# Performance work log

Measured on AMD Instinct MI355X. Metric: run time of the kernel, lower is better.

## Reference

```python
import jax, jax.numpy as jnp
import numpy as np

B, C, H, W = 8, 256, 128, 128  # dim=256 channels, match_factor=2 -> num_matching=128


def setup_inputs() -> dict:
    key = jax.random.key(0)
    k1, k2 = jax.random.split(key)
    x = jax.random.normal(k1, (B, C, H, W), dtype=jnp.float32)
    Ym = jax.random.normal(k2, (B, C, H, W), dtype=jnp.float32)
    return {"x": x, "Ym": Ym, "num_matching": 128}


def _matching(x, Ym, num_matching):
    # x, Ym: (B, C, H, W); flatten spatial -> (B, C, N) with N = H*W
    b, c, h, w = x.shape
    xf = x.reshape(b, c, h * w)
    yf = Ym.reshape(b, c, h * w)
    # pairwise L2 distances between channel vectors: (B, C, C)
    x2 = jnp.sum(xf * xf, axis=-1)
    y2 = jnp.sum(yf * yf, axis=-1)
    d2 = x2[:, :, None] + y2[:, None, :] - 2.0 * jnp.einsum('bin,bjn->bij', xf, yf)
    dist = jnp.sqrt(jnp.maximum(d2, 0.0))
    # topk(k=1, largest=False) == min / argmin over candidates
    topk_values = jnp.min(dist, axis=-1)      # (B, C)
    topk_indices = jnp.argmin(dist, axis=-1)  # (B, C) nearest candidate per input channel
    # keep the num_matching input channels with smallest min-distance, in original order
    order = jnp.argsort(topk_values, axis=1)[:, :num_matching]  # channel ids with rank < num_matching
    sel = jnp.sort(order, axis=1)                               # restore original channel order (masked_select semantics)
    nn_idx = jnp.take_along_axis(topk_indices, sel, axis=1)     # (B, num_matching)
    # batched gather of candidate rows: (B, num_matching, N)
    filt = jnp.take_along_axis(yf, nn_idx[:, :, None], axis=1)
    return filt.reshape(b, num_matching, h, w)


def reference(x, Ym, num_matching):
    return _matching(x, Ym, num_matching)
```

## Files before the change

kernel.cpp:

```cpp
#include <hip/hip_runtime.h>

#define B_  8
#define C_  256
#define N_  16384
#define NM_ 128

typedef _Float16 f16x8 __attribute__((ext_vector_type(8)));
typedef float    f32x4 __attribute__((ext_vector_type(4)));

#define MFMA16(A, Bf, Cc) __builtin_amdgcn_mfma_f32_16x16x32_f16((A), (Bf), (Cc), 0, 0, 0)
#define AS1 __attribute__((address_space(1)))
#define AS3 __attribute__((address_space(3)))

#define CVT(P0, P1, HI, LO, SQ)                           \
    {                                                     \
        float tmp_[8];                                    \
        *(f32x4*)&tmp_[0] = (P0);                         \
        *(f32x4*)&tmp_[4] = (P1);                         \
        _Pragma("unroll")                                 \
        for (int e_ = 0; e_ < 8; ++e_) {                  \
            float v_ = tmp_[e_];                          \
            _Float16 h_ = (_Float16)v_;                   \
            (HI)[e_] = h_;                                \
            (LO)[e_] = (_Float16)(v_ - (float)h_);        \
            (SQ) += v_ * v_;                              \
        }                                                 \
    }

__global__ __launch_bounds__(512)
__attribute__((amdgpu_waves_per_eu(2, 2)))
void gemm_f16_kernel(const float* __restrict__ X,
                     const float* __restrict__ Y,
                     float* __restrict__ Gp,
                     float* __restrict__ x2p,
                     float* __restrict__ y2p,
                     int Kchunk) {
    __shared__ float A_lds[3][256 * 32];
    __shared__ float B_lds[3][128 * 32];

    int cpx = gridDim.x >> 3;
    int lin = (blockIdx.x & 7) * cpx + (blockIdx.x >> 3);

    int jt = lin & 1, b = (lin >> 1) & 7, ks = lin >> 4;
    int k0 = ks * Kchunk;
    int nsteps = Kchunk >> 5;

    int t = threadIdx.x;
    int lane = t & 63;
    int wid = t >> 6;
    int wm = wid >> 1, wn = wid & 1;
    int fr = lane & 15, ug = lane >> 4;

    const float* Xb = X + (size_t)(b * C_) * N_;
    const float* Yb = Y + (size_t)(b * C_ + jt * 128) * N_;

    int lrow = lane >> 3;
    int lchk = lane & 7;
    int lhalf = lchk & 1;
    int luni = lchk >> 1;

    f32x4 acc[4][4] = {};
    float sA[4] = {0.f, 0.f, 0.f, 0.f};
    float sB[4] = {0.f, 0.f, 0.f, 0.f};

    auto issue = [&](int chunk, int sl) {
        int kbase = k0 + chunk * 32;
#pragma unroll
        for (int q = 0; q < 4; ++q) {
            int r = wid * 32 + q * 8 + lrow;
            int kA = ((luni ^ (r & 3)) << 3) + lhalf * 4;
            __builtin_amdgcn_global_load_lds(
                (const AS1 void*)(Xb + (size_t)r * N_ + kbase + kA),
                (AS3 void*)&A_lds[sl][(wid * 32 + q * 8) * 32], 16, 0, 0);
        }
#pragma unroll
        for (int q = 0; q < 2; ++q) {
            int r = wid * 16 + q * 8 + lrow;
            int kB = ((luni ^ (r & 3)) << 3) + lhalf * 4;
            __builtin_amdgcn_global_load_lds(
                (const AS1 void*)(Yb + (size_t)r * N_ + kbase + kB),
                (AS3 void*)&B_lds[sl][(wid * 16 + q * 8) * 32], 16, 0, 0);
        }
    };

    issue(0, 0);
    issue(1, 1);
    asm volatile("s_waitcnt vmcnt(6)" ::: "memory");
    __builtin_amdgcn_s_barrier();
    __builtin_amdgcn_sched_barrier(0);

    for (int i = 0; i < nsteps; ++i) {
        int sl = i % 3;
        if (i + 2 < nsteps) issue(i + 2, (i + 2) % 3);
        __builtin_amdgcn_sched_barrier(0);

        f16x8 aHi[4], aLo[4];
#pragma unroll
        for (int mf = 0; mf < 4; ++mf) {
            int r = wm * 64 + mf * 16 + fr;
            const float* p = &A_lds[sl][r * 32 + ((ug ^ (r & 3)) << 3)];
            f32x4 p0 = *(const f32x4*)p;
            f32x4 p1 = *(const f32x4*)(p + 4);
            CVT(p0, p1, aHi[mf], aLo[mf], sA[mf]);
        }
#pragma unroll
        for (int nf = 0; nf < 4; ++nf) {
            int r = wn * 64 + nf * 16 + fr;
            const float* p = &B_lds[sl][r * 32 + ((ug ^ (r & 3)) << 3)];
            f32x4 q0 = *(const f32x4*)p;
            f32x4 q1 = *(const f32x4*)(p + 4);
            f16x8 bHi, bLo;
            CVT(q0, q1, bHi, bLo, sB[nf]);
            __builtin_amdgcn_s_setprio(1);
            acc[0][nf] = MFMA16(aHi[0], bHi, acc[0][nf]);
            acc[1][nf] = MFMA16(aHi[1], bHi, acc[1][nf]);
            acc[2][nf] = MFMA16(aHi[2], bHi, acc[2][nf]);
            acc[3][nf] = MFMA16(aHi[3], bHi, acc[3][nf]);
            acc[0][nf] = MFMA16(aHi[0], bLo, acc[0][nf]);
            acc[1][nf] = MFMA16(aHi[1], bLo, acc[1][nf]);
            acc[2][nf] = MFMA16(aHi[2], bLo, acc[2][nf]);
            acc[3][nf] = MFMA16(aHi[3], bLo, acc[3][nf]);
            acc[0][nf] = MFMA16(aLo[0], bHi, acc[0][nf]);
            acc[1][nf] = MFMA16(aLo[1], bHi, acc[1][nf]);
            acc[2][nf] = MFMA16(aLo[2], bHi, acc[2][nf]);
            acc[3][nf] = MFMA16(aLo[3], bHi, acc[3][nf]);
            __builtin_amdgcn_s_setprio(0);
        }

        __builtin_amdgcn_sched_barrier(0);
        if (i + 2 < nsteps) {
            asm volatile("s_waitcnt vmcnt(6)" ::: "memory");
        } else {
            asm volatile("s_waitcnt vmcnt(0)" ::: "memory");
        }
        __builtin_amdgcn_s_barrier();
        __builtin_amdgcn_sched_barrier(0);
    }

#pragma unroll
    for (int mf = 0; mf < 4; ++mf) {
        float s = sA[mf];
        s += __shfl_xor(s, 16);
        s += __shfl_xor(s, 32);
        if (jt == 0 && wn == 0 && lane < 16)
            x2p[(ks * B_ + b) * C_ + wm * 64 + mf * 16 + lane] = s;
    }
#pragma unroll
    for (int nf = 0; nf < 4; ++nf) {
        float s = sB[nf];
        s += __shfl_xor(s, 16);
        s += __shfl_xor(s, 32);
        if (wm == 0 && lane < 16)
            y2p[(ks * B_ + b) * C_ + jt * 128 + wn * 64 + nf * 16 + lane] = s;
    }

    size_t gbase = (size_t)(ks * B_ + b) * C_ * C_ + (size_t)jt * 128;
#pragma unroll
    for (int mf = 0; mf < 4; ++mf)
#pragma unroll
        for (int nf = 0; nf < 4; ++nf) {
            int rr = wm * 64 + mf * 16 + (lane >> 4) * 4;
            int cc = wn * 64 + nf * 16 + (lane & 15);
#pragma unroll
            for (int r = 0; r < 4; ++r)
                Gp[gbase + (size_t)(rr + r) * C_ + cc] = acc[mf][nf][r];
        }
}

__global__ __launch_bounds__(256) void argmin_kernel(const float* __restrict__ Gp,
                                                     const float* __restrict__ x2p,
                                                     const float* __restrict__ y2p,
                                                     float* __restrict__ minval,
                                                     int* __restrict__ minidx,
                                                     int KS) {
    int bi = blockIdx.x;
    int b = bi >> 8;
    int i = bi & 255;
    int j = threadIdx.x;

    float g = 0.f, sx = 0.f, sy = 0.f;
    for (int ks = 0; ks < KS; ++ks) {
        g  += Gp[((size_t)(ks * B_ + b) * C_ + i) * C_ + j];
        sx += x2p[(ks * B_ + b) * C_ + i];
        sy += y2p[(ks * B_ + b) * C_ + j];
    }

    float v = sx + sy - 2.f * g;
    int idx = j;
#pragma unroll
    for (int off = 32; off > 0; off >>= 1) {
        float v2 = __shfl_down(v, off);
        int i2 = __shfl_down(idx, off);
        if (v2 < v || (v2 == v && i2 < idx)) { v = v2; idx = i2; }
    }
    __shared__ float wv[4];
    __shared__ int wi[4];
    int lane = threadIdx.x & 63, wid = threadIdx.x >> 6;
    if (lane == 0) { wv[wid] = v; wi[wid] = idx; }
    __syncthreads();
    if (threadIdx.x == 0) {
        for (int w = 1; w < 4; ++w)
            if (wv[w] < v || (wv[w] == v && wi[w] < idx)) { v = wv[w]; idx = wi[w]; }
        minval[bi] = v;
        minidx[bi] = idx;
    }
}

__global__ __launch_bounds__(256) void select_kernel(const float* __restrict__ minval,
                                                     const int* __restrict__ minidx,
                                                     int* __restrict__ nn) {
    int b = blockIdx.x;
    int i = threadIdx.x;
    __shared__ float vals[C_];
    __shared__ int wcnt[4];

    float v = minval[b * C_ + i];
    vals[i] = v;
    __syncthreads();

    int rank = 0;
    for (int tt = 0; tt < C_; ++tt) {
        float u = vals[tt];
        rank += (u < v) || (u == v && tt < i);
    }
    bool flag = rank < NM_;

    unsigned long long m = __ballot(flag);
    int lane = i & 63, wid = i >> 6;
    if (lane == 0) wcnt[wid] = (int)__popcll(m);
    __syncthreads();
    int off = 0;
    for (int w = 0; w < wid; ++w) off += wcnt[w];
    int pos = off + (int)__popcll(m & ((1ULL << lane) - 1ULL));
    if (flag) nn[b * NM_ + pos] = minidx[b * C_ + i];
}

__global__ __launch_bounds__(256) void gather_kernel(const float* __restrict__ Y,
                                                     const int* __restrict__ nn,
                                                     float* __restrict__ out) {
    int blk = blockIdx.x;
    int b = blk >> 7;
    int m = blk & 127;
    int src = nn[b * NM_ + m];
    const float4* s = (const float4*)(Y + ((size_t)b * C_ + src) * N_);
    float4* d = (float4*)(out + ((size_t)b * NM_ + m) * N_);
    for (int tt = threadIdx.x; tt < N_ / 4; tt += 256) d[tt] = s[tt];
}

extern "C" void kernel_launch(void* const* d_in, const int* in_sizes, int n_in,
                              void* d_out, int out_size, void* d_ws, size_t ws_size,
                              hipStream_t stream) {
    const float* X = (const float*)d_in[0];
    const float* Y = (const float*)d_in[1];
    float* out = (float*)d_out;

    size_t favail = ws_size / 4;
    int KS = 1;
    while (KS < 16) {
        int KS2 = KS * 2;
        size_t need = (size_t)KS2 * B_ * C_ * C_
                    + (size_t)KS2 * 2 * B_ * C_
                    + 2 * B_ * C_ + B_ * NM_;
        if (need > favail) break;
        KS = KS2;
    }
    int Kchunk = N_ / KS;

    float* minval = (float*)d_ws;
    int* minidx = (int*)(minval + B_ * C_);
    int* nn = minidx + B_ * C_;
    float* x2p = (float*)(nn + B_ * NM_);
    float* y2p = x2p + (size_t)KS * B_ * C_;
    float* Gp = y2p + (size_t)KS * B_ * C_;

    hipLaunchKernelGGL(gemm_f16_kernel, dim3(KS * 16), dim3(512), 0, stream, X, Y, Gp, x2p, y2p, Kchunk);
    hipLaunchKernelGGL(argmin_kernel, dim3(B_ * C_), dim3(256), 0, stream, Gp, x2p, y2p, minval, minidx, KS);
    hipLaunchKernelGGL(select_kernel, dim3(B_), dim3(256), 0, stream, minval, minidx, nn);
    hipLaunchKernelGGL(gather_kernel, dim3(B_ * NM_), dim3(256), 0, stream, Y, nn, out);
}
```

Baseline: 146.5 us.

## Split GEMM into 128x128 tiles with 256-thread blocks and double buffering

Result: faster. 130.6 us (-10.9%).

```diff
diff --git a/kernel.cpp b/kernel.cpp
--- a/kernel.cpp
+++ b/kernel.cpp
@@ -27,7 +27,7 @@
         }                                                 \
     }
 
-__global__ __launch_bounds__(512)
+__global__ __launch_bounds__(256)
 __attribute__((amdgpu_waves_per_eu(2, 2)))
 void gemm_f16_kernel(const float* __restrict__ X,
                      const float* __restrict__ Y,
@@ -35,13 +35,13 @@
                      float* __restrict__ x2p,
                      float* __restrict__ y2p,
                      int Kchunk) {
-    __shared__ float A_lds[3][256 * 32];
-    __shared__ float B_lds[3][128 * 32];
+    __shared__ float A_lds[2][128 * 32];
+    __shared__ float B_lds[2][128 * 32];
 
     int cpx = gridDim.x >> 3;
     int lin = (blockIdx.x & 7) * cpx + (blockIdx.x >> 3);
 
-    int jt = lin & 1, b = (lin >> 1) & 7, ks = lin >> 4;
+    int jt = lin & 1, it = (lin >> 1) & 1, b = (lin >> 2) & 7, ks = lin >> 5;
     int k0 = ks * Kchunk;
     int nsteps = Kchunk >> 5;
 
@@ -51,13 +51,12 @@
     int wm = wid >> 1, wn = wid & 1;
     int fr = lane & 15, ug = lane >> 4;
 
-    const float* Xb = X + (size_t)(b * C_) * N_;
+    const float* Xb = X + (size_t)(b * C_ + it * 128) * N_;
     const float* Yb = Y + (size_t)(b * C_ + jt * 128) * N_;
 
     int lrow = lane >> 3;
     int lchk = lane & 7;
-    int lhalf = lchk & 1;
-    int luni = lchk >> 1;
+    int lsw = (lchk ^ lrow) << 2;
 
     f32x4 acc[4][4] = {};
     float sA[4] = {0.f, 0.f, 0.f, 0.f};
@@ -68,47 +67,43 @@
 #pragma unroll
         for (int q = 0; q < 4; ++q) {
             int r = wid * 32 + q * 8 + lrow;
-            int kA = ((luni ^ (r & 3)) << 3) + lhalf * 4;
             __builtin_amdgcn_global_load_lds(
-                (const AS1 void*)(Xb + (size_t)r * N_ + kbase + kA),
+                (const AS1 void*)(Xb + (size_t)r * N_ + kbase + lsw),
                 (AS3 void*)&A_lds[sl][(wid * 32 + q * 8) * 32], 16, 0, 0);
         }
 #pragma unroll
-        for (int q = 0; q < 2; ++q) {
-            int r = wid * 16 + q * 8 + lrow;
-            int kB = ((luni ^ (r & 3)) << 3) + lhalf * 4;
+        for (int q = 0; q < 4; ++q) {
+            int r = wid * 32 + q * 8 + lrow;
             __builtin_amdgcn_global_load_lds(
-                (const AS1 void*)(Yb + (size_t)r * N_ + kbase + kB),
-                (AS3 void*)&B_lds[sl][(wid * 16 + q * 8) * 32], 16, 0, 0);
+                (const AS1 void*)(Yb + (size_t)r * N_ + kbase + lsw),
+                (AS3 void*)&B_lds[sl][(wid * 32 + q * 8) * 32], 16, 0, 0);
         }
     };
 
     issue(0, 0);
-    issue(1, 1);
-    asm volatile("s_waitcnt vmcnt(6)" ::: "memory");
+    if (nsteps > 1) issue(1, 1);
+    asm volatile("s_waitcnt vmcnt(8)" ::: "memory");
     __builtin_amdgcn_s_barrier();
     __builtin_amdgcn_sched_barrier(0);
 
     for (int i = 0; i < nsteps; ++i) {
-        int sl = i % 3;
-        if (i + 2 < nsteps) issue(i + 2, (i + 2) % 3);
-        __builtin_amdgcn_sched_barrier(0);
+        int sl = i & 1;
 
         f16x8 aHi[4], aLo[4];
 #pragma unroll
         for (int mf = 0; mf < 4; ++mf) {
             int r = wm * 64 + mf * 16 + fr;
-            const float* p = &A_lds[sl][r * 32 + ((ug ^ (r & 3)) << 3)];
-            f32x4 p0 = *(const f32x4*)p;
-            f32x4 p1 = *(const f32x4*)(p + 4);
+            int s7 = r & 7;
+            f32x4 p0 = *(const f32x4*)&A_lds[sl][r * 32 + (((ug * 2)     ^ s7) << 2)];
+            f32x4 p1 = *(const f32x4*)&A_lds[sl][r * 32 + (((ug * 2 + 1) ^ s7) << 2)];
             CVT(p0, p1, aHi[mf], aLo[mf], sA[mf]);
         }
 #pragma unroll
         for (int nf = 0; nf < 4; ++nf) {
             int r = wn * 64 + nf * 16 + fr;
-            const float* p = &B_lds[sl][r * 32 + ((ug ^ (r & 3)) << 3)];
-            f32x4 q0 = *(const f32x4*)p;
-            f32x4 q1 = *(const f32x4*)(p + 4);
+            int s7 = r & 7;
+            f32x4 q0 = *(const f32x4*)&B_lds[sl][r * 32 + (((ug * 2)     ^ s7) << 2)];
+            f32x4 q1 = *(const f32x4*)&B_lds[sl][r * 32 + (((ug * 2 + 1) ^ s7) << 2)];
             f16x8 bHi, bLo;
             CVT(q0, q1, bHi, bLo, sB[nf]);
             __builtin_amdgcn_s_setprio(1);
@@ -129,12 +124,15 @@
 
         __builtin_amdgcn_sched_barrier(0);
         if (i + 2 < nsteps) {
-            asm volatile("s_waitcnt vmcnt(6)" ::: "memory");
+            asm volatile("s_waitcnt vmcnt(0)" ::: "memory");
+            __builtin_amdgcn_s_barrier();
+            __builtin_amdgcn_sched_barrier(0);
+            issue(i + 2, sl);
         } else {
             asm volatile("s_waitcnt vmcnt(0)" ::: "memory");
-        }
-        __builtin_amdgcn_s_barrier();
-        __builtin_amdgcn_sched_barrier(0);
+            __builtin_amdgcn_s_barrier();
+            __builtin_amdgcn_sched_barrier(0);
+        }
     }
 
 #pragma unroll
@@ -143,18 +141,18 @@
         s += __shfl_xor(s, 16);
         s += __shfl_xor(s, 32);
         if (jt == 0 && wn == 0 && lane < 16)
-            x2p[(ks * B_ + b) * C_ + wm * 64 + mf * 16 + lane] = s;
+            x2p[(ks * B_ + b) * C_ + it * 128 + wm * 64 + mf * 16 + lane] = s;
     }
 #pragma unroll
     for (int nf = 0; nf < 4; ++nf) {
         float s = sB[nf];
         s += __shfl_xor(s, 16);
         s += __shfl_xor(s, 32);
-        if (wm == 0 && lane < 16)
+        if (it == 0 && wm == 0 && lane < 16)
             y2p[(ks * B_ + b) * C_ + jt * 128 + wn * 64 + nf * 16 + lane] = s;
     }
 
-    size_t gbase = (size_t)(ks * B_ + b) * C_ * C_ + (size_t)jt * 128;
+    size_t gbase = ((size_t)(ks * B_ + b) * C_ + it * 128) * C_ + jt * 128;
 #pragma unroll
     for (int mf = 0; mf < 4; ++mf)
 #pragma unroll
@@ -273,7 +271,7 @@
     float* y2p = x2p + (size_t)KS * B_ * C_;
     float* Gp = y2p + (size_t)KS * B_ * C_;
 
-    hipLaunchKernelGGL(gemm_f16_kernel, dim3(KS * 16), dim3(512), 0, stream, X, Y, Gp, x2p, y2p, Kchunk);
+    hipLaunchKernelGGL(gemm_f16_kernel, dim3(KS * 32), dim3(256), 0, stream, X, Y, Gp, x2p, y2p, Kchunk);
     hipLaunchKernelGGL(argmin_kernel, dim3(B_ * C_), dim3(256), 0, stream, Gp, x2p, y2p, minval, minidx, KS);
     hipLaunchKernelGGL(select_kernel, dim3(B_), dim3(256), 0, stream, minval, minidx, nn);
     hipLaunchKernelGGL(gather_kernel, dim3(B_ * NM_), dim3(256), 0, stream, Y, nn, out);
```
